# Kernel tuning notes

Hardware: AMD Instinct MI355X
Metric: run time of the kernel (lower is better)

Reference implementation:

```python
import jax, jax.numpy as jnp
import numpy as np

NUM_NODES = 100000
EMB_DIM = 64
NUM_EDGES = 1280000
NUM_LAYERS = 3


def setup_inputs() -> dict:
    key = jax.random.key(0)
    k1, k2 = jax.random.split(key)
    edge_index = jax.random.randint(k1, (2, NUM_EDGES), 0, NUM_NODES, dtype=jnp.int32)
    emb = jax.random.normal(k2, (NUM_NODES, EMB_DIM), dtype=jnp.float32) * 0.01
    return {"edge_index": edge_index, "emb": emb}


def _lgconv_norm(edge_index):
    # PyG gcn_norm without self-loops: deg over destination nodes,
    # norm_e = deg[src]^-0.5 * deg[dst]^-0.5
    src, dst = edge_index[0], edge_index[1]
    deg = jax.ops.segment_sum(jnp.ones((edge_index.shape[1],), jnp.float32), dst,
                              num_segments=NUM_NODES)
    dinv = jnp.where(deg > 0, jax.lax.rsqrt(jnp.maximum(deg, 1.0)), 0.0)
    return src, dst, dinv[src] * dinv[dst]


def reference(edge_index, emb):
    src, dst, w = _lgconv_norm(edge_index)
    x = emb
    out = x
    for _ in range(NUM_LAYERS):
        # message: gather source embeddings, scale, scatter-add to destination
        x = jax.ops.segment_sum(x[src] * w[:, None], dst, num_segments=NUM_NODES)
        out = out + x
    return out / (NUM_LAYERS + 1)
```

## Files before the change

### kernel.cpp

```cpp
#include <hip/hip_runtime.h>

#define N_NODES 100000
#define EMB 64
#define N_EDGES 1280000
#define N_E4 (N_EDGES / 4)
#define SCAN_TILE 1024

#define NBUCK 196
#define BUCK_SHIFT 9
#define BUCK_NODES 512
#define EPB 4096
#define NBA 313
#define HTOT (NBUCK * NBA)
#define NBH ((HTOT + 1023) / 1024)

typedef unsigned long long u64;
typedef _Float16 f16;
typedef __attribute__((ext_vector_type(2))) _Float16 f16x2;

__global__ void bucket_hist_kernel(const int* __restrict__ dst, int* __restrict__ hist) {
    __shared__ int lh[NBUCK];
    for (int i = threadIdx.x; i < NBUCK; i += 256) lh[i] = 0;
    __syncthreads();
#pragma unroll
    for (int k = 0; k < 4; ++k) {
        int q = blockIdx.x * 1024 + k * 256 + threadIdx.x;
        if (q < N_E4) {
            int4 d4 = ((const int4*)dst)[q];
            atomicAdd(&lh[d4.x >> BUCK_SHIFT], 1);
            atomicAdd(&lh[d4.y >> BUCK_SHIFT], 1);
            atomicAdd(&lh[d4.z >> BUCK_SHIFT], 1);
            atomicAdd(&lh[d4.w >> BUCK_SHIFT], 1);
        }
    }
    __syncthreads();
    for (int i = threadIdx.x; i < NBUCK; i += 256)
        hist[i * NBA + blockIdx.x] = lh[i];
}

__global__ void hist_scan1_kernel(int* __restrict__ hist, int* __restrict__ hbs) {
    __shared__ int lds[256];
    int base = blockIdx.x * 1024;
    int vals[4];
    int tsum = 0;
#pragma unroll
    for (int k = 0; k < 4; ++k) {
        int i = base + threadIdx.x * 4 + k;
        vals[k] = (i < HTOT) ? hist[i] : 0;
        tsum += vals[k];
    }
    lds[threadIdx.x] = tsum;
    __syncthreads();
    for (int off = 1; off < 256; off <<= 1) {
        int v = (threadIdx.x >= (unsigned)off) ? lds[threadIdx.x - off] : 0;
        __syncthreads();
        lds[threadIdx.x] += v;
        __syncthreads();
    }
    int run = lds[threadIdx.x] - tsum;
    if (threadIdx.x == 255) hbs[blockIdx.x] = lds[255];
    #pragma unroll
    for (int k = 0; k < 4; ++k) {
        int i = base + threadIdx.x * 4 + k;
        if (i < HTOT) hist[i] = run;
        run += vals[k];
    }
}

__global__ void hist_scan2_kernel(int* __restrict__ hbs) {
    __shared__ int lds[64];
    int v = (threadIdx.x < (unsigned)NBH) ? hbs[threadIdx.x] : 0;
    lds[threadIdx.x] = v;
    __syncthreads();
    for (int off = 1; off < 64; off <<= 1) {
        int t = (threadIdx.x >= (unsigned)off) ? lds[threadIdx.x - off] : 0;
        __syncthreads();
        lds[threadIdx.x] += t;
        __syncthreads();
    }
    if (threadIdx.x < (unsigned)NBH) hbs[threadIdx.x] = lds[threadIdx.x] - v;
}

__global__ void bucket_scatter_kernel(const int* __restrict__ src, const int* __restrict__ dst,
                                      const int* __restrict__ hist, const int* __restrict__ hbs,
                                      int* __restrict__ bsrc, int* __restrict__ bdst) {
    __shared__ int cur[NBUCK];
    for (int i = threadIdx.x; i < NBUCK; i += 256) {
        int idx = i * NBA + blockIdx.x;
        cur[i] = hist[idx] + hbs[idx >> 10];
    }
    __syncthreads();
#pragma unroll
    for (int k = 0; k < 4; ++k) {
        int q = blockIdx.x * 1024 + k * 256 + threadIdx.x;
        if (q < N_E4) {
            int4 d4 = ((const int4*)dst)[q];
            int4 s4 = ((const int4*)src)[q];
            int p;
            p = atomicAdd(&cur[d4.x >> BUCK_SHIFT], 1); bsrc[p] = s4.x; bdst[p] = d4.x;
            p = atomicAdd(&cur[d4.y >> BUCK_SHIFT], 1); bsrc[p] = s4.y; bdst[p] = d4.y;
            p = atomicAdd(&cur[d4.z >> BUCK_SHIFT], 1); bsrc[p] = s4.z; bdst[p] = d4.z;
            p = atomicAdd(&cur[d4.w >> BUCK_SHIFT], 1); bsrc[p] = s4.w; bdst[p] = d4.w;
        }
    }
}

__global__ void bucket_rank_kernel(const int* __restrict__ hist, const int* __restrict__ hbs,
                                   const int* __restrict__ bdst,
                                   int* __restrict__ brank, int* __restrict__ deg) {
    __shared__ int lh[BUCK_NODES];
    int k = blockIdx.x;
    int i0 = k * NBA;
    int beg = hist[i0] + hbs[i0 >> 10];
    int end;
    if (k + 1 < NBUCK) {
        int i1 = (k + 1) * NBA;
        end = hist[i1] + hbs[i1 >> 10];
    } else {
        end = N_EDGES;
    }
    for (int i = threadIdx.x; i < BUCK_NODES; i += 256) lh[i] = 0;
    __syncthreads();
    for (int i = beg + threadIdx.x; i < end; i += 256) {
        int d = bdst[i];
        brank[i] = atomicAdd(&lh[d & (BUCK_NODES - 1)], 1);
    }
    __syncthreads();
    int nbase = k * BUCK_NODES;
    for (int i = threadIdx.x; i < BUCK_NODES; i += 256)
        if (nbase + i < N_NODES) deg[nbase + i] = lh[i];
}

__global__ void csr_fill_kernel(const int* __restrict__ row_start, const int* __restrict__ bdst,
                                const int* __restrict__ brank, const int* __restrict__ bsrc,
                                int* __restrict__ col) {
    int q = blockIdx.x * blockDim.x + threadIdx.x;
    if (q < N_E4) {
        int4 d4 = ((const int4*)bdst)[q];
        int4 r4 = ((const int4*)brank)[q];
        int4 s4 = ((const int4*)bsrc)[q];
        col[row_start[d4.x] + r4.x] = s4.x;
        col[row_start[d4.y] + r4.y] = s4.y;
        col[row_start[d4.z] + r4.z] = s4.z;
        col[row_start[d4.w] + r4.w] = s4.w;
    }
}

__global__ void norm_kernel(const int* __restrict__ deg, float* __restrict__ dinv,
                            float* __restrict__ rdinv) {
    int i = blockIdx.x * blockDim.x + threadIdx.x;
    if (i < N_NODES) {
        int d = deg[i];
        float fd = (float)d;
        dinv[i]  = (d > 0) ? rsqrtf(fd) : 0.0f;
        rdinv[i] = (d > 0) ? sqrtf(fd) : 0.0f;
    }
}

__global__ void y0_kernel(const float* __restrict__ emb, const float* __restrict__ dinv,
                          f16* __restrict__ y0) {
    int i = blockIdx.x * blockDim.x + threadIdx.x;
    const int n4 = N_NODES * EMB / 4;
    if (i < n4) {
        float dv = dinv[i >> 4];
        float4 v = ((const float4*)emb)[i];
        f16 h[4] = {(f16)(v.x * dv), (f16)(v.y * dv), (f16)(v.z * dv), (f16)(v.w * dv)};
        ((u64*)y0)[i] = *(const u64*)h;
    }
}

__global__ void scan1_kernel(const int* __restrict__ deg, int* __restrict__ local_scan,
                             int* __restrict__ block_sums) {
    __shared__ int lds[256];
    int base = blockIdx.x * SCAN_TILE;
    int vals[4];
    int tsum = 0;
#pragma unroll
    for (int k = 0; k < 4; ++k) {
        int i = base + threadIdx.x * 4 + k;
        vals[k] = (i < N_NODES) ? deg[i] : 0;
        tsum += vals[k];
    }
    lds[threadIdx.x] = tsum;
    __syncthreads();
    for (int off = 1; off < 256; off <<= 1) {
        int v = (threadIdx.x >= (unsigned)off) ? lds[threadIdx.x - off] : 0;
        __syncthreads();
        lds[threadIdx.x] += v;
        __syncthreads();
    }
    int texcl = lds[threadIdx.x] - tsum;
    if (threadIdx.x == 255) block_sums[blockIdx.x] = lds[255];
    int run = texcl;
#pragma unroll
    for (int k = 0; k < 4; ++k) {
        int i = base + threadIdx.x * 4 + k;
        if (i < N_NODES) local_scan[i] = run;
        run += vals[k];
    }
}

__global__ void scan2_kernel(int* __restrict__ block_sums, int nb) {
    __shared__ int lds[128];
    int v = (threadIdx.x < (unsigned)nb) ? block_sums[threadIdx.x] : 0;
    lds[threadIdx.x] = v;
    __syncthreads();
    for (int off = 1; off < 128; off <<= 1) {
        int t = (threadIdx.x >= (unsigned)off) ? lds[threadIdx.x - off] : 0;
        __syncthreads();
        lds[threadIdx.x] += t;
        __syncthreads();
    }
    if (threadIdx.x < (unsigned)nb) block_sums[threadIdx.x] = lds[threadIdx.x] - v;
}

__global__ void scan3_kernel(int* __restrict__ row_start, const int* __restrict__ block_sums) {
    int i = blockIdx.x * blockDim.x + threadIdx.x;
    if (i < N_NODES) {
        row_start[i] = row_start[i] + block_sums[i / SCAN_TILE];
    }
    if (i == 0) row_start[N_NODES] = N_EDGES;
}

template <bool FINAL>
__global__ void gather_kernel(const int* __restrict__ row_start, const int* __restrict__ col,
                              const float* __restrict__ dinv, const float* __restrict__ rdinv,
                              const f16* __restrict__ yin, f16* __restrict__ yout,
                              const float* __restrict__ emb,
                              const f16* __restrict__ y1, const f16* __restrict__ y2,
                              float* __restrict__ out) {
    unsigned int gid = blockIdx.x * blockDim.x + threadIdx.x;
    unsigned int row = gid >> 6;
    int lane = (int)(gid & 63u);
    int s = lane >> 5;
    int j = lane & 31;
    if (row >= N_NODES) return;
    int beg = row_start[row];
    int end = row_start[row + 1];
    const f16* yj = yin + 2 * j;
    float accx = 0.0f, accy = 0.0f;
    for (int cb = beg; cb < end; cb += 64) {
        int idx = cb + lane;
        int ci = 0;
        if (idx < end) ci = col[idx];
        int n = end - cb;
        if (n > 64) n = 64;
        int kk = 0;
        for (; kk + 8 <= n; kk += 8) {
            int c0 = __shfl(ci, kk + s);
            int c1 = __shfl(ci, kk + s + 2);
            int c2 = __shfl(ci, kk + s + 4);
            int c3 = __shfl(ci, kk + s + 6);
            unsigned u0 = *(const unsigned*)(yj + (unsigned)c0 * EMB);
            unsigned u1 = *(const unsigned*)(yj + (unsigned)c1 * EMB);
            unsigned u2 = *(const unsigned*)(yj + (unsigned)c2 * EMB);
            unsigned u3 = *(const unsigned*)(yj + (unsigned)c3 * EMB);
            f16x2 h0 = __builtin_bit_cast(f16x2, u0);
            f16x2 h1 = __builtin_bit_cast(f16x2, u1);
            f16x2 h2 = __builtin_bit_cast(f16x2, u2);
            f16x2 h3 = __builtin_bit_cast(f16x2, u3);
            accx += (float)h0.x + (float)h1.x + (float)h2.x + (float)h3.x;
            accy += (float)h0.y + (float)h1.y + (float)h2.y + (float)h3.y;
        }
        if (kk + 4 <= n) {
            int c0 = __shfl(ci, kk + s);
            int c1 = __shfl(ci, kk + s + 2);
            unsigned u0 = *(const unsigned*)(yj + (unsigned)c0 * EMB);
            unsigned u1 = *(const unsigned*)(yj + (unsigned)c1 * EMB);
            f16x2 h0 = __builtin_bit_cast(f16x2, u0);
            f16x2 h1 = __builtin_bit_cast(f16x2, u1);
            accx += (float)h0.x + (float)h1.x;
            accy += (float)h0.y + (float)h1.y;
            kk += 4;
        }
        for (; kk < n; ++kk) {
            int c = __shfl(ci, kk);
            if (s == (kk & 1)) {
                unsigned u = *(const unsigned*)(yj + (unsigned)c * EMB);
                f16x2 h = __builtin_bit_cast(f16x2, u);
                accx += (float)h.x;
                accy += (float)h.y;
            }
        }
    }
    accx += __shfl_xor(accx, 32);
    accy += __shfl_xor(accy, 32);
    if (s == 0) {
        float dv = dinv[row];
        unsigned int o = row * EMB + 2 * (unsigned)j;
        if (!FINAL) {
            float sc = dv * dv;
            f16x2 h;
            h.x = (f16)(accx * sc);
            h.y = (f16)(accy * sc);
            *(unsigned*)(yout + o) = __builtin_bit_cast(unsigned, h);
        } else {
            float rv = rdinv[row];
            float2 e2 = *(const float2*)(emb + o);
            f16x2 a = __builtin_bit_cast(f16x2, *(const unsigned*)(y1 + o));
            f16x2 b = __builtin_bit_cast(f16x2, *(const unsigned*)(y2 + o));
            float rx = 0.25f * (e2.x + rv * ((float)a.x + (float)b.x) + dv * accx);
            float ry = 0.25f * (e2.y + rv * ((float)a.y + (float)b.y) + dv * accy);
            __builtin_nontemporal_store(rx, out + o);
            __builtin_nontemporal_store(ry, out + o + 1);
        }
    }
}

extern "C" void kernel_launch(void* const* d_in, const int* in_sizes, int n_in,
                              void* d_out, int out_size, void* d_ws, size_t ws_size,
                              hipStream_t stream) {
    const int*   edge = (const int*)d_in[0];
    const int*   src  = edge;
    const int*   dst  = edge + N_EDGES;
    const float* emb  = (const float*)d_in[1];
    float*       out  = (float*)d_out;

    char* ws = (char*)d_ws;
    size_t off = 0;
    int* deg       = (int*)(ws + off); off += 400000;
    int* row_start = (int*)(ws + off); off += 400016;
    int* bsums     = (int*)(ws + off); off += 512;
    int* hbs       = (int*)(ws + off); off += 256;
    float* dinv    = (float*)(ws + off); off += 400000;
    float* rdinv   = (float*)(ws + off); off += 400000;
    int* hist      = (int*)(ws + off); off += (size_t)HTOT * 4 + 16;
    int* col       = (int*)(ws + off); off += (size_t)N_EDGES * 4;
    f16* y0        = (f16*)(ws + off); off += (size_t)N_NODES * EMB * 2;
    f16* y1        = (f16*)(ws + off); off += (size_t)N_NODES * EMB * 2;
    f16* y2        = (f16*)(ws + off); off += (size_t)N_NODES * EMB * 2;

    int* bsrc  = (int*)y1;
    int* bdst  = (int*)((char*)y1 + (size_t)N_EDGES * 4);
    int* brank = (int*)y2;

    const int NB = (N_NODES + SCAN_TILE - 1) / SCAN_TILE;

    bucket_hist_kernel<<<NBA, 256, 0, stream>>>(dst, hist);
    hist_scan1_kernel<<<NBH, 256, 0, stream>>>(hist, hbs);
    hist_scan2_kernel<<<1, 64, 0, stream>>>(hbs);
    bucket_scatter_kernel<<<NBA, 256, 0, stream>>>(src, dst, hist, hbs, bsrc, bdst);
    bucket_rank_kernel<<<NBUCK, 256, 0, stream>>>(hist, hbs, bdst, brank, deg);
    norm_kernel<<<(N_NODES + 255) / 256, 256, 0, stream>>>(deg, dinv, rdinv);
    y0_kernel<<<(N_NODES * EMB / 4 + 255) / 256, 256, 0, stream>>>(emb, dinv, y0);
    scan1_kernel<<<NB, 256, 0, stream>>>(deg, row_start, bsums);
    scan2_kernel<<<1, 128, 0, stream>>>(bsums, NB);
    scan3_kernel<<<(N_NODES + 255) / 256, 256, 0, stream>>>(row_start, bsums);
    csr_fill_kernel<<<(N_E4 + 255) / 256, 256, 0, stream>>>(row_start, bdst, brank,
                                                            bsrc, col);

    const unsigned int gthreads = (unsigned int)N_NODES * EMB;
    const int gblocks = (int)((gthreads + 255) / 256);
    gather_kernel<false><<<gblocks, 256, 0, stream>>>(row_start, col, dinv, rdinv,
                                                      y0, y1, emb, y1, y2, out);
    gather_kernel<false><<<gblocks, 256, 0, stream>>>(row_start, col, dinv, rdinv,
                                                      y1, y2, emb, y1, y2, out);
    gather_kernel<true><<<gblocks, 256, 0, stream>>>(row_start, col, dinv, rdinv,
                                                     y2, (f16*)0, emb, y1, y2, out);
}
```

Baseline: 285.6 us.

## Split fp16 embeddings into XCD-mapped 16-wide slices and fuse norm into rank

Stores the fp16 intermediate embeddings as four column slices of 16 features, each contiguous across nodes. Blocks are mapped so each slice pair of XCDs works on one slice, so each XCD's L2 holds only a quarter of the feature table. Each wavefront now covers 8 neighbours in parallel per 8 lanes, with a three-step shuffle reduction. The norm kernel is also folded into bucket_rank, and stores use nontemporal hints. This relies on round-robin block-to-XCD assignment and launches many more small blocks.

```diff
diff --git a/kernel.cpp b/kernel.cpp
--- a/kernel.cpp
+++ b/kernel.cpp
@@ -5,11 +5,11 @@
 #define N_EDGES 1280000
 #define N_E4 (N_EDGES / 4)
 #define SCAN_TILE 1024
+#define SLICE_F16 (N_NODES * 16)
 
 #define NBUCK 196
 #define BUCK_SHIFT 9
 #define BUCK_NODES 512
-#define EPB 4096
 #define NBA 313
 #define HTOT (NBUCK * NBA)
 #define NBH ((HTOT + 1023) / 1024)
@@ -17,6 +17,7 @@
 typedef unsigned long long u64;
 typedef _Float16 f16;
 typedef __attribute__((ext_vector_type(2))) _Float16 f16x2;
+typedef __attribute__((ext_vector_type(2))) float f32x2;
 
 __global__ void bucket_hist_kernel(const int* __restrict__ dst, int* __restrict__ hist) {
     __shared__ int lh[NBUCK];
@@ -107,7 +108,8 @@
 
 __global__ void bucket_rank_kernel(const int* __restrict__ hist, const int* __restrict__ hbs,
                                    const int* __restrict__ bdst,
-                                   int* __restrict__ brank, int* __restrict__ deg) {
+                                   int* __restrict__ brank, int* __restrict__ deg,
+                                   float* __restrict__ dinv, float* __restrict__ rdinv) {
     __shared__ int lh[BUCK_NODES];
     int k = blockIdx.x;
     int i0 = k * NBA;
@@ -127,8 +129,16 @@
     }
     __syncthreads();
     int nbase = k * BUCK_NODES;
-    for (int i = threadIdx.x; i < BUCK_NODES; i += 256)
-        if (nbase + i < N_NODES) deg[nbase + i] = lh[i];
+    for (int i = threadIdx.x; i < BUCK_NODES; i += 256) {
+        int nn = nbase + i;
+        if (nn < N_NODES) {
+            int d = lh[i];
+            deg[nn] = d;
+            float fd = (float)d;
+            dinv[nn]  = (d > 0) ? rsqrtf(fd) : 0.0f;
+            rdinv[nn] = (d > 0) ? sqrtf(fd) : 0.0f;
+        }
+    }
 }
 
 __global__ void csr_fill_kernel(const int* __restrict__ row_start, const int* __restrict__ bdst,
@@ -146,26 +156,26 @@
     }
 }
 
-__global__ void norm_kernel(const int* __restrict__ deg, float* __restrict__ dinv,
-                            float* __restrict__ rdinv) {
-    int i = blockIdx.x * blockDim.x + threadIdx.x;
-    if (i < N_NODES) {
-        int d = deg[i];
-        float fd = (float)d;
-        dinv[i]  = (d > 0) ? rsqrtf(fd) : 0.0f;
-        rdinv[i] = (d > 0) ? sqrtf(fd) : 0.0f;
-    }
-}
-
 __global__ void y0_kernel(const float* __restrict__ emb, const float* __restrict__ dinv,
                           f16* __restrict__ y0) {
-    int i = blockIdx.x * blockDim.x + threadIdx.x;
-    const int n4 = N_NODES * EMB / 4;
-    if (i < n4) {
-        float dv = dinv[i >> 4];
-        float4 v = ((const float4*)emb)[i];
-        f16 h[4] = {(f16)(v.x * dv), (f16)(v.y * dv), (f16)(v.z * dv), (f16)(v.w * dv)};
-        ((u64*)y0)[i] = *(const u64*)h;
+    int t = blockIdx.x * blockDim.x + threadIdx.x;
+    if (t < N_NODES * 4) {
+        int slice = t & 3;
+        int row = t >> 2;
+        float dv = dinv[row];
+        const float4* e = (const float4*)(emb + (size_t)row * EMB + slice * 16);
+        f16 h[16];
+#pragma unroll
+        for (int q = 0; q < 4; ++q) {
+            float4 v = e[q];
+            h[q * 4 + 0] = (f16)(v.x * dv);
+            h[q * 4 + 1] = (f16)(v.y * dv);
+            h[q * 4 + 2] = (f16)(v.z * dv);
+            h[q * 4 + 3] = (f16)(v.w * dv);
+        }
+        int4* o = (int4*)(y0 + (size_t)slice * SLICE_F16 + (size_t)row * 16);
+        o[0] = ((const int4*)h)[0];
+        o[1] = ((const int4*)h)[1];
     }
 }
 
@@ -229,15 +239,17 @@
                               const float* __restrict__ emb,
                               const f16* __restrict__ y1, const f16* __restrict__ y2,
                               float* __restrict__ out) {
-    unsigned int gid = blockIdx.x * blockDim.x + threadIdx.x;
-    unsigned int row = gid >> 6;
-    int lane = (int)(gid & 63u);
-    int s = lane >> 5;
-    int j = lane & 31;
-    if (row >= N_NODES) return;
+    unsigned b = blockIdx.x;
+    int xcd = b & 7;
+    int k = xcd >> 1;
+    int half = xcd & 1;
+    unsigned row = (unsigned)half * (N_NODES / 2) + (b >> 3) * 4 + (threadIdx.x >> 6);
+    int lane = threadIdx.x & 63;
+    int s = lane >> 3;
+    int j = lane & 7;
     int beg = row_start[row];
     int end = row_start[row + 1];
-    const f16* yj = yin + 2 * j;
+    const f16* yj = yin + (size_t)k * SLICE_F16 + 2 * j;
     float accx = 0.0f, accy = 0.0f;
     for (int cb = beg; cb < end; cb += 64) {
         int idx = cb + lane;
@@ -246,63 +258,59 @@
         int n = end - cb;
         if (n > 64) n = 64;
         int kk = 0;
-        for (; kk + 8 <= n; kk += 8) {
+        for (; kk + 16 <= n; kk += 16) {
             int c0 = __shfl(ci, kk + s);
-            int c1 = __shfl(ci, kk + s + 2);
-            int c2 = __shfl(ci, kk + s + 4);
-            int c3 = __shfl(ci, kk + s + 6);
-            unsigned u0 = *(const unsigned*)(yj + (unsigned)c0 * EMB);
-            unsigned u1 = *(const unsigned*)(yj + (unsigned)c1 * EMB);
-            unsigned u2 = *(const unsigned*)(yj + (unsigned)c2 * EMB);
-            unsigned u3 = *(const unsigned*)(yj + (unsigned)c3 * EMB);
-            f16x2 h0 = __builtin_bit_cast(f16x2, u0);
-            f16x2 h1 = __builtin_bit_cast(f16x2, u1);
-            f16x2 h2 = __builtin_bit_cast(f16x2, u2);
-            f16x2 h3 = __builtin_bit_cast(f16x2, u3);
-            accx += (float)h0.x + (float)h1.x + (float)h2.x + (float)h3.x;
-            accy += (float)h0.y + (float)h1.y + (float)h2.y + (float)h3.y;
-        }
-        if (kk + 4 <= n) {
-            int c0 = __shfl(ci, kk + s);
-            int c1 = __shfl(ci, kk + s + 2);
-            unsigned u0 = *(const unsigned*)(yj + (unsigned)c0 * EMB);
-            unsigned u1 = *(const unsigned*)(yj + (unsigned)c1 * EMB);
+            int c1 = __shfl(ci, kk + 8 + s);
+            unsigned u0 = *(const unsigned*)(yj + (unsigned)c0 * 16);
+            unsigned u1 = *(const unsigned*)(yj + (unsigned)c1 * 16);
             f16x2 h0 = __builtin_bit_cast(f16x2, u0);
             f16x2 h1 = __builtin_bit_cast(f16x2, u1);
             accx += (float)h0.x + (float)h1.x;
             accy += (float)h0.y + (float)h1.y;
-            kk += 4;
-        }
-        for (; kk < n; ++kk) {
-            int c = __shfl(ci, kk);
-            if (s == (kk & 1)) {
-                unsigned u = *(const unsigned*)(yj + (unsigned)c * EMB);
-                f16x2 h = __builtin_bit_cast(f16x2, u);
-                accx += (float)h.x;
-                accy += (float)h.y;
+        }
+        if (kk + 8 <= n) {
+            int c0 = __shfl(ci, kk + s);
+            unsigned u0 = *(const unsigned*)(yj + (unsigned)c0 * 16);
+            f16x2 h0 = __builtin_bit_cast(f16x2, u0);
+            accx += (float)h0.x;
+            accy += (float)h0.y;
+            kk += 8;
+        }
+        if (kk < n) {
+            int c0 = __shfl(ci, (kk + s) & 63);
+            if (kk + s < n) {
+                unsigned u0 = *(const unsigned*)(yj + (unsigned)c0 * 16);
+                f16x2 h0 = __builtin_bit_cast(f16x2, u0);
+                accx += (float)h0.x;
+                accy += (float)h0.y;
             }
         }
     }
-    accx += __shfl_xor(accx, 32);
-    accy += __shfl_xor(accy, 32);
+    accx += __shfl_xor(accx, 8);  accy += __shfl_xor(accy, 8);
+    accx += __shfl_xor(accx, 16); accy += __shfl_xor(accy, 16);
+    accx += __shfl_xor(accx, 32); accy += __shfl_xor(accy, 32);
     if (s == 0) {
         float dv = dinv[row];
-        unsigned int o = row * EMB + 2 * (unsigned)j;
+        unsigned so = (unsigned)k * SLICE_F16 + row * 16 + 2 * (unsigned)j;
         if (!FINAL) {
             float sc = dv * dv;
             f16x2 h;
             h.x = (f16)(accx * sc);
             h.y = (f16)(accy * sc);
-            *(unsigned*)(yout + o) = __builtin_bit_cast(unsigned, h);
+            unsigned hv = __builtin_bit_cast(unsigned, h);
+            __builtin_nontemporal_store(hv, (unsigned*)(yout + so));
         } else {
             float rv = rdinv[row];
-            float2 e2 = *(const float2*)(emb + o);
-            f16x2 a = __builtin_bit_cast(f16x2, *(const unsigned*)(y1 + o));
-            f16x2 b = __builtin_bit_cast(f16x2, *(const unsigned*)(y2 + o));
-            float rx = 0.25f * (e2.x + rv * ((float)a.x + (float)b.x) + dv * accx);
-            float ry = 0.25f * (e2.y + rv * ((float)a.y + (float)b.y) + dv * accy);
-            __builtin_nontemporal_store(rx, out + o);
-            __builtin_nontemporal_store(ry, out + o + 1);
+            unsigned od = row * EMB + (unsigned)k * 16 + 2 * (unsigned)j;
+            f32x2 e2 = __builtin_nontemporal_load((const f32x2*)(emb + od));
+            unsigned ua = __builtin_nontemporal_load((const unsigned*)(y1 + so));
+            unsigned ub = __builtin_nontemporal_load((const unsigned*)(y2 + so));
+            f16x2 a = __builtin_bit_cast(f16x2, ua);
+            f16x2 bb = __builtin_bit_cast(f16x2, ub);
+            float rx = 0.25f * (e2.x + rv * ((float)a.x + (float)bb.x) + dv * accx);
+            float ry = 0.25f * (e2.y + rv * ((float)a.y + (float)bb.y) + dv * accy);
+            __builtin_nontemporal_store(rx, out + od);
+            __builtin_nontemporal_store(ry, out + od + 1);
         }
     }
 }
@@ -340,17 +348,16 @@
     hist_scan1_kernel<<<NBH, 256, 0, stream>>>(hist, hbs);
     hist_scan2_kernel<<<1, 64, 0, stream>>>(hbs);
     bucket_scatter_kernel<<<NBA, 256, 0, stream>>>(src, dst, hist, hbs, bsrc, bdst);
-    bucket_rank_kernel<<<NBUCK, 256, 0, stream>>>(hist, hbs, bdst, brank, deg);
-    norm_kernel<<<(N_NODES + 255) / 256, 256, 0, stream>>>(deg, dinv, rdinv);
-    y0_kernel<<<(N_NODES * EMB / 4 + 255) / 256, 256, 0, stream>>>(emb, dinv, y0);
+    bucket_rank_kernel<<<NBUCK, 256, 0, stream>>>(hist, hbs, bdst, brank, deg,
+                                                  dinv, rdinv);
+    y0_kernel<<<(N_NODES * 4 + 255) / 256, 256, 0, stream>>>(emb, dinv, y0);
     scan1_kernel<<<NB, 256, 0, stream>>>(deg, row_start, bsums);
     scan2_kernel<<<1, 128, 0, stream>>>(bsums, NB);
     scan3_kernel<<<(N_NODES + 255) / 256, 256, 0, stream>>>(row_start, bsums);
     csr_fill_kernel<<<(N_E4 + 255) / 256, 256, 0, stream>>>(row_start, bdst, brank,
                                                             bsrc, col);
 
-    const unsigned int gthreads = (unsigned int)N_NODES * EMB;
-    const int gblocks = (int)((gthreads + 255) / 256);
+    const int gblocks = N_NODES;
     gather_kernel<false><<<gblocks, 256, 0, stream>>>(row_start, col, dinv, rdinv,
                                                       y0, y1, emb, y1, y2, out);
     gather_kernel<false><<<gblocks, 256, 0, stream>>>(row_start, col, dinv, rdinv,
```

After: 452.4 us. 58.4% more time.

## Pack bucketed edges and build CSR per bucket in one kernel

Applied to the files above, without the earlier changes.

The bucket scatter now packs the source id and the local destination offset into a single 32-bit word, which halves the intermediate edge traffic. A new per-bucket kernel builds the local degree histogram, scans it in LDS to get row_start, computes dinv/rdinv, and fills col with LDS atomics. This replaces the rank, norm, three-stage scan and csr_fill kernels. It removes several launches and the global scattered col writes, but relies on bucket ranges being globally contiguous and on node ids fitting in 17 bits.

```diff
diff --git a/kernel.cpp b/kernel.cpp
--- a/kernel.cpp
+++ b/kernel.cpp
@@ -4,12 +4,10 @@
 #define EMB 64
 #define N_EDGES 1280000
 #define N_E4 (N_EDGES / 4)
-#define SCAN_TILE 1024
 
 #define NBUCK 196
 #define BUCK_SHIFT 9
 #define BUCK_NODES 512
-#define EPB 4096
 #define NBA 313
 #define HTOT (NBUCK * NBA)
 #define NBH ((HTOT + 1023) / 1024)
@@ -83,7 +81,7 @@
 
 __global__ void bucket_scatter_kernel(const int* __restrict__ src, const int* __restrict__ dst,
                                       const int* __restrict__ hist, const int* __restrict__ hbs,
-                                      int* __restrict__ bsrc, int* __restrict__ bdst) {
+                                      int* __restrict__ bedge) {
     __shared__ int cur[NBUCK];
     for (int i = threadIdx.x; i < NBUCK; i += 256) {
         int idx = i * NBA + blockIdx.x;
@@ -97,19 +95,27 @@
             int4 d4 = ((const int4*)dst)[q];
             int4 s4 = ((const int4*)src)[q];
             int p;
-            p = atomicAdd(&cur[d4.x >> BUCK_SHIFT], 1); bsrc[p] = s4.x; bdst[p] = d4.x;
-            p = atomicAdd(&cur[d4.y >> BUCK_SHIFT], 1); bsrc[p] = s4.y; bdst[p] = d4.y;
-            p = atomicAdd(&cur[d4.z >> BUCK_SHIFT], 1); bsrc[p] = s4.z; bdst[p] = d4.z;
-            p = atomicAdd(&cur[d4.w >> BUCK_SHIFT], 1); bsrc[p] = s4.w; bdst[p] = d4.w;
-        }
-    }
-}
-
-__global__ void bucket_rank_kernel(const int* __restrict__ hist, const int* __restrict__ hbs,
-                                   const int* __restrict__ bdst,
-                                   int* __restrict__ brank, int* __restrict__ deg) {
+            p = atomicAdd(&cur[d4.x >> BUCK_SHIFT], 1);
+            bedge[p] = s4.x | ((d4.x & (BUCK_NODES - 1)) << 17);
+            p = atomicAdd(&cur[d4.y >> BUCK_SHIFT], 1);
+            bedge[p] = s4.y | ((d4.y & (BUCK_NODES - 1)) << 17);
+            p = atomicAdd(&cur[d4.z >> BUCK_SHIFT], 1);
+            bedge[p] = s4.z | ((d4.z & (BUCK_NODES - 1)) << 17);
+            p = atomicAdd(&cur[d4.w >> BUCK_SHIFT], 1);
+            bedge[p] = s4.w | ((d4.w & (BUCK_NODES - 1)) << 17);
+        }
+    }
+}
+
+__global__ void bucket_build_kernel(const int* __restrict__ hist, const int* __restrict__ hbs,
+                                    const int* __restrict__ bedge,
+                                    int* __restrict__ col, int* __restrict__ row_start,
+                                    float* __restrict__ dinv, float* __restrict__ rdinv) {
     __shared__ int lh[BUCK_NODES];
+    __shared__ int sc[256];
+    __shared__ int cur[BUCK_NODES];
     int k = blockIdx.x;
+    int tid = threadIdx.x;
     int i0 = k * NBA;
     int beg = hist[i0] + hbs[i0 >> 10];
     int end;
@@ -119,41 +125,43 @@
     } else {
         end = N_EDGES;
     }
-    for (int i = threadIdx.x; i < BUCK_NODES; i += 256) lh[i] = 0;
-    __syncthreads();
-    for (int i = beg + threadIdx.x; i < end; i += 256) {
-        int d = bdst[i];
-        brank[i] = atomicAdd(&lh[d & (BUCK_NODES - 1)], 1);
-    }
-    __syncthreads();
-    int nbase = k * BUCK_NODES;
-    for (int i = threadIdx.x; i < BUCK_NODES; i += 256)
-        if (nbase + i < N_NODES) deg[nbase + i] = lh[i];
-}
-
-__global__ void csr_fill_kernel(const int* __restrict__ row_start, const int* __restrict__ bdst,
-                                const int* __restrict__ brank, const int* __restrict__ bsrc,
-                                int* __restrict__ col) {
-    int q = blockIdx.x * blockDim.x + threadIdx.x;
-    if (q < N_E4) {
-        int4 d4 = ((const int4*)bdst)[q];
-        int4 r4 = ((const int4*)brank)[q];
-        int4 s4 = ((const int4*)bsrc)[q];
-        col[row_start[d4.x] + r4.x] = s4.x;
-        col[row_start[d4.y] + r4.y] = s4.y;
-        col[row_start[d4.z] + r4.z] = s4.z;
-        col[row_start[d4.w] + r4.w] = s4.w;
-    }
-}
-
-__global__ void norm_kernel(const int* __restrict__ deg, float* __restrict__ dinv,
-                            float* __restrict__ rdinv) {
-    int i = blockIdx.x * blockDim.x + threadIdx.x;
-    if (i < N_NODES) {
-        int d = deg[i];
-        float fd = (float)d;
-        dinv[i]  = (d > 0) ? rsqrtf(fd) : 0.0f;
-        rdinv[i] = (d > 0) ? sqrtf(fd) : 0.0f;
+    lh[tid] = 0;
+    lh[tid + 256] = 0;
+    __syncthreads();
+    for (int i = beg + tid; i < end; i += 256)
+        atomicAdd(&lh[((unsigned)bedge[i]) >> 17], 1);
+    __syncthreads();
+    int v0 = lh[2 * tid];
+    int v1 = lh[2 * tid + 1];
+    int tsum = v0 + v1;
+    sc[tid] = tsum;
+    __syncthreads();
+    for (int off = 1; off < 256; off <<= 1) {
+        int v = (tid >= off) ? sc[tid - off] : 0;
+        __syncthreads();
+        sc[tid] += v;
+        __syncthreads();
+    }
+    int texcl = sc[tid] - tsum;
+    cur[2 * tid] = texcl;
+    cur[2 * tid + 1] = texcl + v0;
+    __syncthreads();
+    for (int i = tid; i < BUCK_NODES; i += 256) {
+        int node = k * BUCK_NODES + i;
+        if (node <= N_NODES) {
+            row_start[node] = beg + cur[i];
+            if (node < N_NODES) {
+                int d = lh[i];
+                float fd = (float)d;
+                dinv[node]  = (d > 0) ? rsqrtf(fd) : 0.0f;
+                rdinv[node] = (d > 0) ? sqrtf(fd) : 0.0f;
+            }
+        }
+    }
+    for (int i = beg + tid; i < end; i += 256) {
+        unsigned pe = (unsigned)bedge[i];
+        int r = atomicAdd(&cur[pe >> 17], 1);
+        col[beg + r] = (int)(pe & 0x1FFFFu);
     }
 }
 
@@ -167,59 +175,6 @@
         f16 h[4] = {(f16)(v.x * dv), (f16)(v.y * dv), (f16)(v.z * dv), (f16)(v.w * dv)};
         ((u64*)y0)[i] = *(const u64*)h;
     }
-}
-
-__global__ void scan1_kernel(const int* __restrict__ deg, int* __restrict__ local_scan,
-                             int* __restrict__ block_sums) {
-    __shared__ int lds[256];
-    int base = blockIdx.x * SCAN_TILE;
-    int vals[4];
-    int tsum = 0;
-#pragma unroll
-    for (int k = 0; k < 4; ++k) {
-        int i = base + threadIdx.x * 4 + k;
-        vals[k] = (i < N_NODES) ? deg[i] : 0;
-        tsum += vals[k];
-    }
-    lds[threadIdx.x] = tsum;
-    __syncthreads();
-    for (int off = 1; off < 256; off <<= 1) {
-        int v = (threadIdx.x >= (unsigned)off) ? lds[threadIdx.x - off] : 0;
-        __syncthreads();
-        lds[threadIdx.x] += v;
-        __syncthreads();
-    }
-    int texcl = lds[threadIdx.x] - tsum;
-    if (threadIdx.x == 255) block_sums[blockIdx.x] = lds[255];
-    int run = texcl;
-#pragma unroll
-    for (int k = 0; k < 4; ++k) {
-        int i = base + threadIdx.x * 4 + k;
-        if (i < N_NODES) local_scan[i] = run;
-        run += vals[k];
-    }
-}
-
-__global__ void scan2_kernel(int* __restrict__ block_sums, int nb) {
-    __shared__ int lds[128];
-    int v = (threadIdx.x < (unsigned)nb) ? block_sums[threadIdx.x] : 0;
-    lds[threadIdx.x] = v;
-    __syncthreads();
-    for (int off = 1; off < 128; off <<= 1) {
-        int t = (threadIdx.x >= (unsigned)off) ? lds[threadIdx.x - off] : 0;
-        __syncthreads();
-        lds[threadIdx.x] += t;
-        __syncthreads();
-    }
-    if (threadIdx.x < (unsigned)nb) block_sums[threadIdx.x] = lds[threadIdx.x] - v;
-}
-
-__global__ void scan3_kernel(int* __restrict__ row_start, const int* __restrict__ block_sums) {
-    int i = blockIdx.x * blockDim.x + threadIdx.x;
-    if (i < N_NODES) {
-        row_start[i] = row_start[i] + block_sums[i / SCAN_TILE];
-    }
-    if (i == 0) row_start[N_NODES] = N_EDGES;
 }
 
 template <bool FINAL>
@@ -318,9 +273,7 @@
 
     char* ws = (char*)d_ws;
     size_t off = 0;
-    int* deg       = (int*)(ws + off); off += 400000;
     int* row_start = (int*)(ws + off); off += 400016;
-    int* bsums     = (int*)(ws + off); off += 512;
     int* hbs       = (int*)(ws + off); off += 256;
     float* dinv    = (float*)(ws + off); off += 400000;
     float* rdinv   = (float*)(ws + off); off += 400000;
@@ -330,24 +283,15 @@
     f16* y1        = (f16*)(ws + off); off += (size_t)N_NODES * EMB * 2;
     f16* y2        = (f16*)(ws + off); off += (size_t)N_NODES * EMB * 2;
 
-    int* bsrc  = (int*)y1;
-    int* bdst  = (int*)((char*)y1 + (size_t)N_EDGES * 4);
-    int* brank = (int*)y2;
-
-    const int NB = (N_NODES + SCAN_TILE - 1) / SCAN_TILE;
+    int* bedge = (int*)y1;
 
     bucket_hist_kernel<<<NBA, 256, 0, stream>>>(dst, hist);
     hist_scan1_kernel<<<NBH, 256, 0, stream>>>(hist, hbs);
     hist_scan2_kernel<<<1, 64, 0, stream>>>(hbs);
-    bucket_scatter_kernel<<<NBA, 256, 0, stream>>>(src, dst, hist, hbs, bsrc, bdst);
-    bucket_rank_kernel<<<NBUCK, 256, 0, stream>>>(hist, hbs, bdst, brank, deg);
-    norm_kernel<<<(N_NODES + 255) / 256, 256, 0, stream>>>(deg, dinv, rdinv);
+    bucket_scatter_kernel<<<NBA, 256, 0, stream>>>(src, dst, hist, hbs, bedge);
+    bucket_build_kernel<<<NBUCK, 256, 0, stream>>>(hist, hbs, bedge, col, row_start,
+                                                   dinv, rdinv);
     y0_kernel<<<(N_NODES * EMB / 4 + 255) / 256, 256, 0, stream>>>(emb, dinv, y0);
-    scan1_kernel<<<NB, 256, 0, stream>>>(deg, row_start, bsums);
-    scan2_kernel<<<1, 128, 0, stream>>>(bsums, NB);
-    scan3_kernel<<<(N_NODES + 255) / 256, 256, 0, stream>>>(row_start, bsums);
-    csr_fill_kernel<<<(N_E4 + 255) / 256, 256, 0, stream>>>(row_start, bdst, brank,
-                                                            bsrc, col);
 
     const unsigned int gthreads = (unsigned int)N_NODES * EMB;
     const int gblocks = (int)((gthreads + 255) / 256);
```

New measurement: 259.7 us. 1.1x faster.
